# Optimization experiments

Hardware: AMD Instinct MI355X
Metric: run time of the kernel (lower is better)

## Reference

```python
import jax, jax.numpy as jnp
import numpy as np

N = 100000      # nodes
E = 3200000     # edges
F_IN = 512      # input features
HID = 16        # hidden (hardcoded in module)
OUT = 1         # out_channels


def setup_inputs() -> dict:
    key = jax.random.key(0)
    k1, k2, k3, k4, k5, k6 = jax.random.split(key, 6)
    x = jax.random.normal(k1, (N, F_IN), dtype=jnp.float32)
    edge_index = jax.random.randint(k2, (2, E), 0, N, dtype=jnp.int32)
    # glorot-ish init for weights, zero bias (PyG GCNConv default: glorot W, zeros b)
    W1 = jax.random.normal(k3, (F_IN, HID), dtype=jnp.float32) * (1.0 / np.sqrt(F_IN))
    b1 = jnp.zeros((HID,), dtype=jnp.float32)
    W2 = jax.random.normal(k4, (HID, OUT), dtype=jnp.float32) * (1.0 / np.sqrt(HID))
    b2 = jnp.zeros((OUT,), dtype=jnp.float32)
    return {"x": x, "W1": W1, "b1": b1, "W2": W2, "b2": b2, "edge_index": edge_index}


def _gcn_conv(x, W, b, src, dst):
    """PyG GCNConv: h = x@W; add self-loops; out_i = sum_j deg_i^-1/2 deg_j^-1/2 h_j + b."""
    h = x @ W  # [N, F_out]
    n = x.shape[0]
    loop = jnp.arange(n, dtype=src.dtype)
    src_sl = jnp.concatenate([src, loop])  # [E+N]
    dst_sl = jnp.concatenate([dst, loop])
    deg = jax.ops.segment_sum(jnp.ones_like(dst_sl, dtype=h.dtype), dst_sl, num_segments=n)
    dinv = jnp.where(deg > 0, jax.lax.rsqrt(deg), 0.0)
    norm = dinv[src_sl] * dinv[dst_sl]  # [E+N]
    msg = h[src_sl] * norm[:, None]     # gather + scale
    out = jax.ops.segment_sum(msg, dst_sl, num_segments=n)  # scatter-add
    return out + b


def reference(x, W1, b1, W2, b2, edge_index):
    src, dst = edge_index[0], edge_index[1]  # flow: source_to_target
    h = jax.nn.relu(_gcn_conv(x, W1, b1, src, dst))
    # dropout(p=0.3) is identity in eval mode
    out = jax.nn.sigmoid(_gcn_conv(h, W2, b2, src, dst))
    return out
```

## Files before the change

### kernel.cpp

```cpp
#include <hip/hip_runtime.h>
#include <math.h>

#define N_NODES 100000
#define N_EDGES 3200000
#define F_IN    512
#define HID     16

#define ROWS_PER_CHUNK 8
#define NCHUNK (N_NODES / ROWS_PER_CHUNK)
#define GEMM1_BLOCKS 512

typedef const __attribute__((address_space(1))) void g_void;
typedef __attribute__((address_space(3))) void l_void;

__global__ void k_deg(const int* __restrict__ dst, float* __restrict__ deg) {
    int e = blockIdx.x * blockDim.x + threadIdx.x;
    if (e < N_EDGES) atomicAdd(&deg[dst[e]], 1.0f);
}

__global__ void k_dinv(const float* __restrict__ deg, float* __restrict__ dinv) {
    int i = blockIdx.x * blockDim.x + threadIdx.x;
    if (i < N_NODES) dinv[i] = rsqrtf(deg[i] + 1.0f);
}

__global__ __launch_bounds__(256, 2)
void k_gemm1(const float* __restrict__ x, const float* __restrict__ W1,
             const float* __restrict__ dinv, float* __restrict__ hs1,
             float* __restrict__ acc1) {
    __shared__ float xs[2 * ROWS_PER_CHUNK * F_IN];
    const int tid  = threadIdx.x;
    const int lane = tid & 63;
    const int wib  = tid >> 6;
    const int q    = lane >> 4;
    const int k    = lane & 15;

    float w[128];
    {
        const float* wp = W1 + (size_t)(q * 128) * HID + k;
#pragma unroll
        for (int j = 0; j < 128; ++j) w[j] = wp[(size_t)j * HID];
    }

    int chunk = blockIdx.x;
    int par = 0;
    {
        const float* gb = x + (size_t)chunk * (ROWS_PER_CHUNK * F_IN);
#pragma unroll
        for (int j = 0; j < 4; ++j) {
            int cidx = j * 4 + wib;
            __builtin_amdgcn_global_load_lds(
                (g_void*)(gb + cidx * 256 + lane * 4),
                (l_void*)(xs + cidx * 256),
                16, 0, 0);
        }
    }

    for (; chunk < NCHUNK; chunk += GEMM1_BLOCKS) {
        const int nxt = chunk + GEMM1_BLOCKS;
        const bool more = (nxt < NCHUNK);
        if (more) {
            const float* gb = x + (size_t)nxt * (ROWS_PER_CHUNK * F_IN);
            float* lb = xs + (par ^ 1) * (ROWS_PER_CHUNK * F_IN);
#pragma unroll
            for (int j = 0; j < 4; ++j) {
                int cidx = j * 4 + wib;
                __builtin_amdgcn_global_load_lds(
                    (g_void*)(gb + cidx * 256 + lane * 4),
                    (l_void*)(lb + cidx * 256),
                    16, 0, 0);
            }
            asm volatile("s_waitcnt vmcnt(4)" ::: "memory");
        } else {
            asm volatile("s_waitcnt vmcnt(0)" ::: "memory");
        }
        __builtin_amdgcn_sched_barrier(0);
        __builtin_amdgcn_s_barrier();
        __builtin_amdgcn_sched_barrier(0);

        const float* xr0 = xs + par * (ROWS_PER_CHUNK * F_IN) + (wib * 2) * F_IN + q * 128;
        const float* xr1 = xr0 + F_IN;
        float a0 = 0.f, c0 = 0.f, a1 = 0.f, c1 = 0.f;
#pragma unroll
        for (int c = 0; c < 32; ++c) {
            float4 v0 = ((const float4*)xr0)[c];
            float4 v1 = ((const float4*)xr1)[c];
            a0 = fmaf(v0.x, w[4 * c + 0], a0);
            c0 = fmaf(v0.y, w[4 * c + 1], c0);
            a0 = fmaf(v0.z, w[4 * c + 2], a0);
            c0 = fmaf(v0.w, w[4 * c + 3], c0);
            a1 = fmaf(v1.x, w[4 * c + 0], a1);
            c1 = fmaf(v1.y, w[4 * c + 1], c1);
            a1 = fmaf(v1.z, w[4 * c + 2], a1);
            c1 = fmaf(v1.w, w[4 * c + 3], c1);
        }
        float s0 = a0 + c0, s1 = a1 + c1;
        s0 += __shfl_xor(s0, 16);
        s0 += __shfl_xor(s0, 32);
        s1 += __shfl_xor(s1, 16);
        s1 += __shfl_xor(s1, 32);
        const int row = chunk * ROWS_PER_CHUNK + wib * 2;
        if (q == 0) {
            float h0 = s0 * dinv[row];
            float h1 = s1 * dinv[row + 1];
            hs1[(size_t)row * HID + k]        = h0;
            acc1[(size_t)row * HID + k]       = h0;
            hs1[(size_t)(row + 1) * HID + k]  = h1;
            acc1[(size_t)(row + 1) * HID + k] = h1;
        }
        __builtin_amdgcn_sched_barrier(0);
        __builtin_amdgcn_s_barrier();
        __builtin_amdgcn_sched_barrier(0);
        par ^= 1;
    }
}

__global__ void k_scatter1(const int* __restrict__ src, const int* __restrict__ dst,
                           const float* __restrict__ hs1, float* __restrict__ acc1) {
    long long t = (long long)blockIdx.x * blockDim.x + threadIdx.x;
    int e = (int)(t >> 4);
    int k = (int)(t & 15);
    if (e < N_EDGES) {
        int s = src[e], d = dst[e];
        atomicAdd(&acc1[(size_t)d * HID + k], hs1[(size_t)s * HID + k]);
    }
}

__global__ void k_mid(const float* __restrict__ acc1, const float* __restrict__ dinv,
                      const float* __restrict__ b1, const float* __restrict__ W2,
                      float* __restrict__ ts, float* __restrict__ acc2) {
    int i = blockIdx.x * blockDim.x + threadIdx.x;
    if (i >= N_NODES) return;
    float di = dinv[i];
    const float4* a = (const float4*)(acc1 + (size_t)i * HID);
    float t = 0.f;
#pragma unroll
    for (int c = 0; c < 4; ++c) {
        float4 v = a[c];
        float z0 = fmaxf(v.x * di + b1[4 * c + 0], 0.f);
        float z1 = fmaxf(v.y * di + b1[4 * c + 1], 0.f);
        float z2 = fmaxf(v.z * di + b1[4 * c + 2], 0.f);
        float z3 = fmaxf(v.w * di + b1[4 * c + 3], 0.f);
        t += z0 * W2[4 * c + 0] + z1 * W2[4 * c + 1] + z2 * W2[4 * c + 2] + z3 * W2[4 * c + 3];
    }
    float v = t * di;
    ts[i]   = v;
    acc2[i] = v;
}

__global__ void k_scatter2(const int* __restrict__ src, const int* __restrict__ dst,
                           const float* __restrict__ ts, float* __restrict__ acc2) {
    int e = blockIdx.x * blockDim.x + threadIdx.x;
    if (e < N_EDGES) atomicAdd(&acc2[dst[e]], ts[src[e]]);
}

__global__ void k_fin(const float* __restrict__ acc2, const float* __restrict__ dinv,
                      const float* __restrict__ b2, float* __restrict__ out) {
    int i = blockIdx.x * blockDim.x + threadIdx.x;
    if (i < N_NODES) {
        float z = acc2[i] * dinv[i] + b2[0];
        out[i] = 1.0f / (1.0f + expf(-z));
    }
}

extern "C" void kernel_launch(void* const* d_in, const int* in_sizes, int n_in,
                              void* d_out, int out_size, void* d_ws, size_t ws_size,
                              hipStream_t stream) {
    const float* x  = (const float*)d_in[0];
    const float* W1 = (const float*)d_in[1];
    const float* b1 = (const float*)d_in[2];
    const float* W2 = (const float*)d_in[3];
    const float* b2 = (const float*)d_in[4];
    const int*   ei = (const int*)d_in[5];
    const int* src = ei;
    const int* dst = ei + N_EDGES;
    float* out = (float*)d_out;

    char* ws = (char*)d_ws;
    float* acc1 = (float*)ws;
    float* hs1  = (float*)(ws + (size_t)N_NODES * HID * 4);
    float* deg  = (float*)(ws + (size_t)2 * N_NODES * HID * 4);
    float* dinv = deg  + N_NODES;
    float* ts   = dinv + N_NODES;
    float* acc2 = ts   + N_NODES;

    hipMemsetAsync(deg, 0, N_NODES * sizeof(float), stream);
    k_deg <<<(N_EDGES + 255) / 256, 256, 0, stream>>>(dst, deg);
    k_dinv<<<(N_NODES + 255) / 256, 256, 0, stream>>>(deg, dinv);
    k_gemm1<<<GEMM1_BLOCKS, 256, 0, stream>>>(x, W1, dinv, hs1, acc1);
    {
        long long tot = (long long)N_EDGES * 16;
        int blocks = (int)((tot + 255) / 256);
        k_scatter1<<<blocks, 256, 0, stream>>>(src, dst, hs1, acc1);
    }
    k_mid <<<(N_NODES + 255) / 256, 256, 0, stream>>>(acc1, dinv, b1, W2, ts, acc2);
    k_scatter2<<<(N_EDGES + 255) / 256, 256, 0, stream>>>(src, dst, ts, acc2);
    k_fin <<<(N_NODES + 255) / 256, 256, 0, stream>>>(acc2, dinv, b2, out);
}
```

Measured before the change: 795.9 us.

## Build CSR by destination and replace atomic scatters with gather aggregation

Builds a destination-sorted CSR (int degree count, two-level prefix scan, atomic-cursor fill) and replaces both edge-parallel atomic scatter-add passes with node-parallel gather kernels. Layer-1 aggregation is fused with bias, ReLU and the W2 projection, and layer-2 aggregation with the sigmoid epilogue. This removes about 51M float atomics and the acc1/acc2 initialisation writes. In exchange it adds a CSR construction pass with random atomic-cursor writes, and load imbalance across nodes with different degrees.

```diff
diff --git a/kernel.cpp b/kernel.cpp
--- a/kernel.cpp
+++ b/kernel.cpp
@@ -6,6 +6,8 @@
 #define F_IN    512
 #define HID     16
 
+#define NB ((N_NODES + 255) / 256)
+
 #define ROWS_PER_CHUNK 8
 #define NCHUNK (N_NODES / ROWS_PER_CHUNK)
 #define GEMM1_BLOCKS 512
@@ -13,20 +15,73 @@
 typedef const __attribute__((address_space(1))) void g_void;
 typedef __attribute__((address_space(3))) void l_void;
 
-__global__ void k_deg(const int* __restrict__ dst, float* __restrict__ deg) {
+__global__ void k_deg(const int* __restrict__ dst, int* __restrict__ deg) {
     int e = blockIdx.x * blockDim.x + threadIdx.x;
-    if (e < N_EDGES) atomicAdd(&deg[dst[e]], 1.0f);
-}
-
-__global__ void k_dinv(const float* __restrict__ deg, float* __restrict__ dinv) {
-    int i = blockIdx.x * blockDim.x + threadIdx.x;
-    if (i < N_NODES) dinv[i] = rsqrtf(deg[i] + 1.0f);
+    if (e < N_EDGES) atomicAdd(&deg[dst[e]], 1);
+}
+
+__global__ void k_bsum(const int* __restrict__ deg, int* __restrict__ bsum) {
+    int i = blockIdx.x * 256 + threadIdx.x;
+    int v = (i < N_NODES) ? deg[i] : 0;
+#pragma unroll
+    for (int o = 1; o < 64; o <<= 1) v += __shfl_xor(v, o);
+    __shared__ int sd[4];
+    if ((threadIdx.x & 63) == 0) sd[threadIdx.x >> 6] = v;
+    __syncthreads();
+    if (threadIdx.x == 0) bsum[blockIdx.x] = sd[0] + sd[1] + sd[2] + sd[3];
+}
+
+__global__ void k_scanb(int* __restrict__ bsum) {
+    __shared__ int s[512];
+    int t = threadIdx.x;
+    int v = (t < NB) ? bsum[t] : 0;
+    s[t] = v;
+    __syncthreads();
+    for (int o = 1; o < 512; o <<= 1) {
+        int u = (t >= o) ? s[t - o] : 0;
+        __syncthreads();
+        s[t] += u;
+        __syncthreads();
+    }
+    if (t < NB) bsum[t] = s[t] - v;
+}
+
+__global__ void k_rowptr(const int* __restrict__ deg, const int* __restrict__ bsum,
+                         int* __restrict__ rowptr, int* __restrict__ cursor,
+                         float* __restrict__ dinv) {
+    __shared__ int s[256];
+    int i = blockIdx.x * 256 + threadIdx.x;
+    int v = (i < N_NODES) ? deg[i] : 0;
+    s[threadIdx.x] = v;
+    __syncthreads();
+    for (int o = 1; o < 256; o <<= 1) {
+        int u = (threadIdx.x >= o) ? s[threadIdx.x - o] : 0;
+        __syncthreads();
+        s[threadIdx.x] += u;
+        __syncthreads();
+    }
+    int excl = s[threadIdx.x] - v;
+    if (i < N_NODES) {
+        int r = bsum[blockIdx.x] + excl;
+        rowptr[i] = r;
+        cursor[i] = r;
+        dinv[i]   = rsqrtf((float)v + 1.0f);
+    }
+    if (i == 0) rowptr[N_NODES] = N_EDGES;
+}
+
+__global__ void k_fill(const int* __restrict__ src, const int* __restrict__ dst,
+                       int* __restrict__ cursor, int* __restrict__ csr) {
+    int e = blockIdx.x * blockDim.x + threadIdx.x;
+    if (e < N_EDGES) {
+        int p = atomicAdd(&cursor[dst[e]], 1);
+        csr[p] = src[e];
+    }
 }
 
 __global__ __launch_bounds__(256, 2)
 void k_gemm1(const float* __restrict__ x, const float* __restrict__ W1,
-             const float* __restrict__ dinv, float* __restrict__ hs1,
-             float* __restrict__ acc1) {
+             const float* __restrict__ dinv, float* __restrict__ hs1) {
     __shared__ float xs[2 * ROWS_PER_CHUNK * F_IN];
     const int tid  = threadIdx.x;
     const int lane = tid & 63;
@@ -50,15 +105,13 @@
             int cidx = j * 4 + wib;
             __builtin_amdgcn_global_load_lds(
                 (g_void*)(gb + cidx * 256 + lane * 4),
-                (l_void*)(xs + cidx * 256),
-                16, 0, 0);
+                (l_void*)(xs + cidx * 256), 16, 0, 0);
         }
     }
 
     for (; chunk < NCHUNK; chunk += GEMM1_BLOCKS) {
         const int nxt = chunk + GEMM1_BLOCKS;
-        const bool more = (nxt < NCHUNK);
-        if (more) {
+        if (nxt < NCHUNK) {
             const float* gb = x + (size_t)nxt * (ROWS_PER_CHUNK * F_IN);
             float* lb = xs + (par ^ 1) * (ROWS_PER_CHUNK * F_IN);
 #pragma unroll
@@ -66,8 +119,7 @@
                 int cidx = j * 4 + wib;
                 __builtin_amdgcn_global_load_lds(
                     (g_void*)(gb + cidx * 256 + lane * 4),
-                    (l_void*)(lb + cidx * 256),
-                    16, 0, 0);
+                    (l_void*)(lb + cidx * 256), 16, 0, 0);
             }
             asm volatile("s_waitcnt vmcnt(4)" ::: "memory");
         } else {
@@ -100,12 +152,8 @@
         s1 += __shfl_xor(s1, 32);
         const int row = chunk * ROWS_PER_CHUNK + wib * 2;
         if (q == 0) {
-            float h0 = s0 * dinv[row];
-            float h1 = s1 * dinv[row + 1];
-            hs1[(size_t)row * HID + k]        = h0;
-            acc1[(size_t)row * HID + k]       = h0;
-            hs1[(size_t)(row + 1) * HID + k]  = h1;
-            acc1[(size_t)(row + 1) * HID + k] = h1;
+            hs1[(size_t)row * HID + k]       = s0 * dinv[row];
+            hs1[(size_t)(row + 1) * HID + k] = s1 * dinv[row + 1];
         }
         __builtin_amdgcn_sched_barrier(0);
         __builtin_amdgcn_s_barrier();
@@ -114,51 +162,50 @@
     }
 }
 
-__global__ void k_scatter1(const int* __restrict__ src, const int* __restrict__ dst,
-                           const float* __restrict__ hs1, float* __restrict__ acc1) {
-    long long t = (long long)blockIdx.x * blockDim.x + threadIdx.x;
-    int e = (int)(t >> 4);
-    int k = (int)(t & 15);
-    if (e < N_EDGES) {
-        int s = src[e], d = dst[e];
-        atomicAdd(&acc1[(size_t)d * HID + k], hs1[(size_t)s * HID + k]);
-    }
-}
-
-__global__ void k_mid(const float* __restrict__ acc1, const float* __restrict__ dinv,
-                      const float* __restrict__ b1, const float* __restrict__ W2,
-                      float* __restrict__ ts, float* __restrict__ acc2) {
-    int i = blockIdx.x * blockDim.x + threadIdx.x;
-    if (i >= N_NODES) return;
-    float di = dinv[i];
-    const float4* a = (const float4*)(acc1 + (size_t)i * HID);
-    float t = 0.f;
-#pragma unroll
-    for (int c = 0; c < 4; ++c) {
-        float4 v = a[c];
-        float z0 = fmaxf(v.x * di + b1[4 * c + 0], 0.f);
-        float z1 = fmaxf(v.y * di + b1[4 * c + 1], 0.f);
-        float z2 = fmaxf(v.z * di + b1[4 * c + 2], 0.f);
-        float z3 = fmaxf(v.w * di + b1[4 * c + 3], 0.f);
-        t += z0 * W2[4 * c + 0] + z1 * W2[4 * c + 1] + z2 * W2[4 * c + 2] + z3 * W2[4 * c + 3];
-    }
-    float v = t * di;
-    ts[i]   = v;
-    acc2[i] = v;
-}
-
-__global__ void k_scatter2(const int* __restrict__ src, const int* __restrict__ dst,
-                           const float* __restrict__ ts, float* __restrict__ acc2) {
-    int e = blockIdx.x * blockDim.x + threadIdx.x;
-    if (e < N_EDGES) atomicAdd(&acc2[dst[e]], ts[src[e]]);
-}
-
-__global__ void k_fin(const float* __restrict__ acc2, const float* __restrict__ dinv,
-                      const float* __restrict__ b2, float* __restrict__ out) {
-    int i = blockIdx.x * blockDim.x + threadIdx.x;
-    if (i < N_NODES) {
-        float z = acc2[i] * dinv[i] + b2[0];
-        out[i] = 1.0f / (1.0f + expf(-z));
+__global__ void k_agg1mid(const float* __restrict__ hs1, const int* __restrict__ rowptr,
+                          const int* __restrict__ csr, const float* __restrict__ dinv,
+                          const float* __restrict__ b1, const float* __restrict__ W2,
+                          float* __restrict__ ts) {
+    int t = blockIdx.x * blockDim.x + threadIdx.x;
+    int g = t >> 4;
+    int k = t & 15;
+    if (g >= N_NODES) return;
+    int beg = rowptr[g], end = rowptr[g + 1];
+    float s0 = hs1[(size_t)g * HID + k];
+    float s1 = 0.f;
+    int e = beg;
+    for (; e + 1 < end; e += 2) {
+        int j0 = csr[e], j1 = csr[e + 1];
+        s0 += hs1[(size_t)j0 * HID + k];
+        s1 += hs1[(size_t)j1 * HID + k];
+    }
+    if (e < end) s0 += hs1[(size_t)csr[e] * HID + k];
+    float di = dinv[g];
+    float z = fmaxf((s0 + s1) * di + b1[k], 0.f) * W2[k];
+    z += __shfl_xor(z, 1, 16);
+    z += __shfl_xor(z, 2, 16);
+    z += __shfl_xor(z, 4, 16);
+    z += __shfl_xor(z, 8, 16);
+    if (k == 0) ts[g] = z * di;
+}
+
+__global__ void k_agg2fin(const float* __restrict__ ts, const int* __restrict__ rowptr,
+                          const int* __restrict__ csr, const float* __restrict__ dinv,
+                          const float* __restrict__ b2, float* __restrict__ out) {
+    int t = blockIdx.x * blockDim.x + threadIdx.x;
+    int g = t >> 4;
+    int l = t & 15;
+    if (g >= N_NODES) return;
+    int beg = rowptr[g], end = rowptr[g + 1];
+    float s = (l == 0) ? ts[g] : 0.f;
+    for (int e = beg + l; e < end; e += 16) s += ts[csr[e]];
+    s += __shfl_xor(s, 1, 16);
+    s += __shfl_xor(s, 2, 16);
+    s += __shfl_xor(s, 4, 16);
+    s += __shfl_xor(s, 8, 16);
+    if (l == 0) {
+        float z = s * dinv[g] + b2[0];
+        out[g] = 1.0f / (1.0f + expf(-z));
     }
 }
 
@@ -176,23 +223,26 @@
     float* out = (float*)d_out;
 
     char* ws = (char*)d_ws;
-    float* acc1 = (float*)ws;
-    float* hs1  = (float*)(ws + (size_t)N_NODES * HID * 4);
-    float* deg  = (float*)(ws + (size_t)2 * N_NODES * HID * 4);
-    float* dinv = deg  + N_NODES;
-    float* ts   = dinv + N_NODES;
-    float* acc2 = ts   + N_NODES;
-
-    hipMemsetAsync(deg, 0, N_NODES * sizeof(float), stream);
-    k_deg <<<(N_EDGES + 255) / 256, 256, 0, stream>>>(dst, deg);
-    k_dinv<<<(N_NODES + 255) / 256, 256, 0, stream>>>(deg, dinv);
-    k_gemm1<<<GEMM1_BLOCKS, 256, 0, stream>>>(x, W1, dinv, hs1, acc1);
+    float* hs1   = (float*)ws;
+    int*   deg    = (int*)(hs1 + (size_t)N_NODES * HID);
+    int*   rowptr = deg + N_NODES;
+    int*   cursor = rowptr + N_NODES + 1;
+    float* dinv   = (float*)(cursor + N_NODES);
+    float* ts     = dinv + N_NODES;
+    int*   bsum   = (int*)(ts + N_NODES);
+    int*   csr    = bsum + 512;
+
+    hipMemsetAsync(deg, 0, N_NODES * sizeof(int), stream);
+    k_deg   <<<(N_EDGES + 255) / 256, 256, 0, stream>>>(dst, deg);
+    k_bsum  <<<NB, 256, 0, stream>>>(deg, bsum);
+    k_scanb <<<1, 512, 0, stream>>>(bsum);
+    k_rowptr<<<NB, 256, 0, stream>>>(deg, bsum, rowptr, cursor, dinv);
+    k_fill  <<<(N_EDGES + 255) / 256, 256, 0, stream>>>(src, dst, cursor, csr);
+    k_gemm1 <<<GEMM1_BLOCKS, 256, 0, stream>>>(x, W1, dinv, hs1);
     {
-        long long tot = (long long)N_EDGES * 16;
+        long long tot = (long long)N_NODES * 16;
         int blocks = (int)((tot + 255) / 256);
-        k_scatter1<<<blocks, 256, 0, stream>>>(src, dst, hs1, acc1);
-    }
-    k_mid <<<(N_NODES + 255) / 256, 256, 0, stream>>>(acc1, dinv, b1, W2, ts, acc2);
-    k_scatter2<<<(N_EDGES + 255) / 256, 256, 0, stream>>>(src, dst, ts, acc2);
-    k_fin <<<(N_NODES + 255) / 256, 256, 0, stream>>>(acc2, dinv, b2, out);
-}
+        k_agg1mid<<<blocks, 256, 0, stream>>>(hs1, rowptr, csr, dinv, b1, W2, ts);
+        k_agg2fin<<<blocks, 256, 0, stream>>>(ts, rowptr, csr, dinv, b2, out);
+    }
+}
```

Result: faster. 762.1 us (-4.2%).

## Bucket edges by destination and aggregate in LDS instead of global atomics

Applied to the files above, without the earlier changes.

Adds a binning pass that packs each edge (src, local dst) into per-destination buckets of 512 nodes while also counting degrees. Both aggregation layers then accumulate in shared-memory atomics per bucket, replacing global atomics. Layer 2 aggregation is fused with the sigmoid epilogue, and self-loop handling moves into k_mid and the epilogue. The aim is to remove heavy contention and random global atomic traffic in the scatter kernels. In exchange it adds an extra pass that writes 3.2M packed edges, and it relies on a fixed bucket capacity (18000) that random inputs must not overflow.

```diff
diff --git a/kernel.cpp b/kernel.cpp
--- a/kernel.cpp
+++ b/kernel.cpp
@@ -6,6 +6,13 @@
 #define F_IN    512
 #define HID     16
 
+#define NBKT     196
+#define BKT_NODES 512
+#define BKT_CAP  18000
+#define BIN_BLOCKS 512
+#define CHUNK_E  1024
+#define NCHUNKS  (N_EDGES / CHUNK_E)
+
 #define ROWS_PER_CHUNK 8
 #define NCHUNK (N_NODES / ROWS_PER_CHUNK)
 #define GEMM1_BLOCKS 512
@@ -13,20 +20,60 @@
 typedef const __attribute__((address_space(1))) void g_void;
 typedef __attribute__((address_space(3))) void l_void;
 
-__global__ void k_deg(const int* __restrict__ dst, float* __restrict__ deg) {
-    int e = blockIdx.x * blockDim.x + threadIdx.x;
-    if (e < N_EDGES) atomicAdd(&deg[dst[e]], 1.0f);
-}
-
-__global__ void k_dinv(const float* __restrict__ deg, float* __restrict__ dinv) {
+__global__ __launch_bounds__(256)
+void k_bin(const int* __restrict__ src, const int* __restrict__ dst,
+           int* __restrict__ deg, int* __restrict__ gcur,
+           unsigned* __restrict__ bins) {
+    __shared__ unsigned stage[NBKT][64];
+    __shared__ int cnt[NBKT];
+    __shared__ int gb[NBKT];
+    const int tid = threadIdx.x;
+
+    for (int c = blockIdx.x; c < NCHUNKS; c += BIN_BLOCKS) {
+        for (int b = tid; b < NBKT; b += 256) cnt[b] = 0;
+        __syncthreads();
+        const int base = c * CHUNK_E;
+#pragma unroll
+        for (int j = 0; j < 4; ++j) {
+            int e = base + j * 256 + tid;
+            int d = dst[e];
+            int s = src[e];
+            atomicAdd(&deg[d], 1);
+            int b = d >> 9;
+            unsigned w = (unsigned)s | ((unsigned)(d & 511) << 17);
+            int p = atomicAdd(&cnt[b], 1);
+            if (p < 64) {
+                stage[b][p] = w;
+            } else {
+                int g = atomicAdd(&gcur[b], 1);
+                bins[(size_t)b * BKT_CAP + g] = w;
+            }
+        }
+        __syncthreads();
+        if (tid < NBKT) {
+            int n = cnt[tid]; if (n > 64) n = 64;
+            cnt[tid] = n;
+            gb[tid] = atomicAdd(&gcur[tid], n);
+        }
+        __syncthreads();
+        const int grp = tid >> 4, ln = tid & 15;
+        for (int b = grp; b < NBKT; b += 16) {
+            int n = cnt[b], g0 = gb[b];
+            for (int j = ln; j < n; j += 16)
+                bins[(size_t)b * BKT_CAP + g0 + j] = stage[b][j];
+        }
+        __syncthreads();
+    }
+}
+
+__global__ void k_dinv(const int* __restrict__ deg, float* __restrict__ dinv) {
     int i = blockIdx.x * blockDim.x + threadIdx.x;
-    if (i < N_NODES) dinv[i] = rsqrtf(deg[i] + 1.0f);
+    if (i < N_NODES) dinv[i] = rsqrtf((float)deg[i] + 1.0f);
 }
 
 __global__ __launch_bounds__(256, 2)
 void k_gemm1(const float* __restrict__ x, const float* __restrict__ W1,
-             const float* __restrict__ dinv, float* __restrict__ hs1,
-             float* __restrict__ acc1) {
+             const float* __restrict__ dinv, float* __restrict__ hs1) {
     __shared__ float xs[2 * ROWS_PER_CHUNK * F_IN];
     const int tid  = threadIdx.x;
     const int lane = tid & 63;
@@ -50,15 +97,13 @@
             int cidx = j * 4 + wib;
             __builtin_amdgcn_global_load_lds(
                 (g_void*)(gb + cidx * 256 + lane * 4),
-                (l_void*)(xs + cidx * 256),
-                16, 0, 0);
+                (l_void*)(xs + cidx * 256), 16, 0, 0);
         }
     }
 
     for (; chunk < NCHUNK; chunk += GEMM1_BLOCKS) {
         const int nxt = chunk + GEMM1_BLOCKS;
-        const bool more = (nxt < NCHUNK);
-        if (more) {
+        if (nxt < NCHUNK) {
             const float* gb = x + (size_t)nxt * (ROWS_PER_CHUNK * F_IN);
             float* lb = xs + (par ^ 1) * (ROWS_PER_CHUNK * F_IN);
 #pragma unroll
@@ -66,8 +111,7 @@
                 int cidx = j * 4 + wib;
                 __builtin_amdgcn_global_load_lds(
                     (g_void*)(gb + cidx * 256 + lane * 4),
-                    (l_void*)(lb + cidx * 256),
-                    16, 0, 0);
+                    (l_void*)(lb + cidx * 256), 16, 0, 0);
             }
             asm volatile("s_waitcnt vmcnt(4)" ::: "memory");
         } else {
@@ -100,12 +144,8 @@
         s1 += __shfl_xor(s1, 32);
         const int row = chunk * ROWS_PER_CHUNK + wib * 2;
         if (q == 0) {
-            float h0 = s0 * dinv[row];
-            float h1 = s1 * dinv[row + 1];
-            hs1[(size_t)row * HID + k]        = h0;
-            acc1[(size_t)row * HID + k]       = h0;
-            hs1[(size_t)(row + 1) * HID + k]  = h1;
-            acc1[(size_t)(row + 1) * HID + k] = h1;
+            hs1[(size_t)row * HID + k]       = s0 * dinv[row];
+            hs1[(size_t)(row + 1) * HID + k] = s1 * dinv[row + 1];
         }
         __builtin_amdgcn_sched_barrier(0);
         __builtin_amdgcn_s_barrier();
@@ -114,51 +154,81 @@
     }
 }
 
-__global__ void k_scatter1(const int* __restrict__ src, const int* __restrict__ dst,
-                           const float* __restrict__ hs1, float* __restrict__ acc1) {
-    long long t = (long long)blockIdx.x * blockDim.x + threadIdx.x;
-    int e = (int)(t >> 4);
-    int k = (int)(t & 15);
-    if (e < N_EDGES) {
-        int s = src[e], d = dst[e];
-        atomicAdd(&acc1[(size_t)d * HID + k], hs1[(size_t)s * HID + k]);
-    }
-}
-
-__global__ void k_mid(const float* __restrict__ acc1, const float* __restrict__ dinv,
-                      const float* __restrict__ b1, const float* __restrict__ W2,
-                      float* __restrict__ ts, float* __restrict__ acc2) {
+__global__ __launch_bounds__(256)
+void k_agg1(const unsigned* __restrict__ bins, const int* __restrict__ gcur,
+            const float* __restrict__ hs1, float* __restrict__ hsum) {
+    __shared__ float acc[BKT_NODES * HID];
+    const int b    = blockIdx.x >> 1;
+    const int half = blockIdx.x & 1;
+    const int tid  = threadIdx.x;
+    for (int j = tid; j < BKT_NODES * HID; j += 256) acc[j] = 0.f;
+    __syncthreads();
+
+    const int n   = gcur[b];
+    const int beg = half ? (n >> 1) : 0;
+    const int end = half ? n : (n >> 1);
+    const unsigned* wp = bins + (size_t)b * BKT_CAP;
+    const int g = tid >> 4, k = tid & 15;
+#pragma unroll 8
+    for (int i = beg + g; i < end; i += 16) {
+        unsigned w = wp[i];
+        int s  = w & 0x1FFFF;
+        int dl = w >> 17;
+        float v = hs1[(size_t)s * HID + k];
+        atomicAdd(&acc[dl * HID + k], v);
+    }
+    __syncthreads();
+    float* hb = hsum + (size_t)b * (BKT_NODES * HID);
+    for (int j = tid; j < BKT_NODES * HID; j += 256) {
+        float v = acc[j];
+        if (v != 0.f) atomicAdd(&hb[j], v);
+    }
+}
+
+__global__ void k_mid(const float* __restrict__ hsum, const float* __restrict__ hs1,
+                      const float* __restrict__ dinv, const float* __restrict__ b1,
+                      const float* __restrict__ W2, float* __restrict__ ts) {
     int i = blockIdx.x * blockDim.x + threadIdx.x;
     if (i >= N_NODES) return;
     float di = dinv[i];
-    const float4* a = (const float4*)(acc1 + (size_t)i * HID);
+    const float4* A = (const float4*)(hsum + (size_t)i * HID);
+    const float4* H = (const float4*)(hs1  + (size_t)i * HID);
     float t = 0.f;
 #pragma unroll
     for (int c = 0; c < 4; ++c) {
-        float4 v = a[c];
-        float z0 = fmaxf(v.x * di + b1[4 * c + 0], 0.f);
-        float z1 = fmaxf(v.y * di + b1[4 * c + 1], 0.f);
-        float z2 = fmaxf(v.z * di + b1[4 * c + 2], 0.f);
-        float z3 = fmaxf(v.w * di + b1[4 * c + 3], 0.f);
+        float4 a = A[c];
+        float4 h = H[c];
+        float z0 = fmaxf((a.x + h.x) * di + b1[4 * c + 0], 0.f);
+        float z1 = fmaxf((a.y + h.y) * di + b1[4 * c + 1], 0.f);
+        float z2 = fmaxf((a.z + h.z) * di + b1[4 * c + 2], 0.f);
+        float z3 = fmaxf((a.w + h.w) * di + b1[4 * c + 3], 0.f);
         t += z0 * W2[4 * c + 0] + z1 * W2[4 * c + 1] + z2 * W2[4 * c + 2] + z3 * W2[4 * c + 3];
     }
-    float v = t * di;
-    ts[i]   = v;
-    acc2[i] = v;
-}
-
-__global__ void k_scatter2(const int* __restrict__ src, const int* __restrict__ dst,
-                           const float* __restrict__ ts, float* __restrict__ acc2) {
-    int e = blockIdx.x * blockDim.x + threadIdx.x;
-    if (e < N_EDGES) atomicAdd(&acc2[dst[e]], ts[src[e]]);
-}
-
-__global__ void k_fin(const float* __restrict__ acc2, const float* __restrict__ dinv,
-                      const float* __restrict__ b2, float* __restrict__ out) {
-    int i = blockIdx.x * blockDim.x + threadIdx.x;
-    if (i < N_NODES) {
-        float z = acc2[i] * dinv[i] + b2[0];
-        out[i] = 1.0f / (1.0f + expf(-z));
+    ts[i] = t * di;
+}
+
+__global__ __launch_bounds__(256)
+void k_agg2fin(const unsigned* __restrict__ bins, const int* __restrict__ gcur,
+               const float* __restrict__ ts, const float* __restrict__ dinv,
+               const float* __restrict__ b2, float* __restrict__ out) {
+    __shared__ float acc[BKT_NODES];
+    const int b = blockIdx.x, tid = threadIdx.x;
+    for (int j = tid; j < BKT_NODES; j += 256) acc[j] = 0.f;
+    __syncthreads();
+    const int n = gcur[b];
+    const unsigned* wp = bins + (size_t)b * BKT_CAP;
+#pragma unroll 8
+    for (int i = tid; i < n; i += 256) {
+        unsigned w = wp[i];
+        atomicAdd(&acc[w >> 17], ts[w & 0x1FFFF]);
+    }
+    __syncthreads();
+    for (int l = tid; l < BKT_NODES; l += 256) {
+        int nd = b * BKT_NODES + l;
+        if (nd < N_NODES) {
+            float z = (ts[nd] + acc[l]) * dinv[nd] + b2[0];
+            out[nd] = 1.0f / (1.0f + expf(-z));
+        }
     }
 }
 
@@ -176,23 +246,21 @@
     float* out = (float*)d_out;
 
     char* ws = (char*)d_ws;
-    float* acc1 = (float*)ws;
-    float* hs1  = (float*)(ws + (size_t)N_NODES * HID * 4);
-    float* deg  = (float*)(ws + (size_t)2 * N_NODES * HID * 4);
-    float* dinv = deg  + N_NODES;
-    float* ts   = dinv + N_NODES;
-    float* acc2 = ts   + N_NODES;
-
-    hipMemsetAsync(deg, 0, N_NODES * sizeof(float), stream);
-    k_deg <<<(N_EDGES + 255) / 256, 256, 0, stream>>>(dst, deg);
-    k_dinv<<<(N_NODES + 255) / 256, 256, 0, stream>>>(deg, dinv);
-    k_gemm1<<<GEMM1_BLOCKS, 256, 0, stream>>>(x, W1, dinv, hs1, acc1);
-    {
-        long long tot = (long long)N_EDGES * 16;
-        int blocks = (int)((tot + 255) / 256);
-        k_scatter1<<<blocks, 256, 0, stream>>>(src, dst, hs1, acc1);
-    }
-    k_mid <<<(N_NODES + 255) / 256, 256, 0, stream>>>(acc1, dinv, b1, W2, ts, acc2);
-    k_scatter2<<<(N_EDGES + 255) / 256, 256, 0, stream>>>(src, dst, ts, acc2);
-    k_fin <<<(N_NODES + 255) / 256, 256, 0, stream>>>(acc2, dinv, b2, out);
-}
+    float*    hs1  = (float*)ws;
+    float*    hsum = hs1 + (size_t)N_NODES * HID;
+    int*      deg  = (int*)(hsum + (size_t)NBKT * BKT_NODES * HID);
+    int*      gcur = deg + N_NODES;
+    float*    dinv = (float*)(gcur + 256);
+    float*    ts   = dinv + N_NODES;
+    unsigned* bins = (unsigned*)(ts + N_NODES);
+
+    hipMemsetAsync(deg, 0, (N_NODES + 256) * sizeof(int), stream);
+    hipMemsetAsync(hsum, 0, (size_t)NBKT * BKT_NODES * HID * sizeof(float), stream);
+
+    k_bin    <<<BIN_BLOCKS, 256, 0, stream>>>(src, dst, deg, gcur, bins);
+    k_dinv   <<<(N_NODES + 255) / 256, 256, 0, stream>>>(deg, dinv);
+    k_gemm1  <<<GEMM1_BLOCKS, 256, 0, stream>>>(x, W1, dinv, hs1);
+    k_agg1   <<<NBKT * 2, 256, 0, stream>>>(bins, gcur, hs1, hsum);
+    k_mid    <<<(N_NODES + 255) / 256, 256, 0, stream>>>(hsum, hs1, dinv, b1, W2, ts);
+    k_agg2fin<<<NBKT, 256, 0, stream>>>(bins, gcur, ts, dinv, b2, out);
+}
```

New measurement: 850.0 us. 1.07x slower.
